# Kernel tuning notes

Hardware: AMD Instinct MI355X
Metric: run time of the kernel (lower is better)

The kernel has to match this reference:

```python
import jax, jax.numpy as jnp
import numpy as np

B, S, D_MODEL, N_HEADS = 4, 2048, 1024, 16
HEAD = D_MODEL // N_HEADS  # 64


def setup_inputs() -> dict:
    key = jax.random.key(0)
    ks = jax.random.split(key, 9)
    s = 1.0 / np.sqrt(D_MODEL)
    return {
        "query": jax.random.normal(ks[0], (B, S, D_MODEL), jnp.float32),
        "key_in": jax.random.normal(ks[1], (B, S, D_MODEL), jnp.float32),
        "value": jax.random.normal(ks[2], (B, S, D_MODEL), jnp.float32),
        "Wq": jax.random.normal(ks[3], (D_MODEL, D_MODEL), jnp.float32) * s,
        "bq": jnp.zeros((D_MODEL,), jnp.float32),
        "Wk": jax.random.normal(ks[4], (D_MODEL, D_MODEL), jnp.float32) * s,
        "bk": jnp.zeros((D_MODEL,), jnp.float32),
        "Wv": jax.random.normal(ks[5], (D_MODEL, D_MODEL), jnp.float32) * s,
        "bv": jnp.zeros((D_MODEL,), jnp.float32),
    }


def reference(query, key_in, value, Wq, bq, Wk, bk, Wv, bv):
    # Dense projections (Keras Dense: x @ W + b)
    q = query @ Wq + bq     # [B,S,D]
    k = key_in @ Wk + bk    # [B,S,D]
    v = value @ Wv + bv     # [B,S,D]
    # split heads -> [B,S,H,Dh]
    q = q.reshape(B, S, N_HEADS, HEAD)
    k = k.reshape(B, S, N_HEADS, HEAD)
    v = v.reshape(B, S, N_HEADS, HEAD)
    scale = 1.0 / jnp.sqrt(jnp.float32(HEAD))
    # full attention matrix [B,H,Sq,Sk] (faithful to original un-fused form)
    scores = jnp.einsum('bqhd,bkhd->bhqk', q, k) * scale
    alpha = jax.nn.softmax(scores, axis=-1)
    ctx = jnp.einsum('bhqk,bkhd->bqhd', alpha, v)  # [B,Sq,H,Dh]
    return ctx.reshape(B, S, D_MODEL)
```

## Files before the change

kernel.cpp:

```cpp
#include <hip/hip_runtime.h>
#include <hip/hip_bf16.h>

#define S_LEN 2048
#define DM    1024
#define NH    16
#define HD    64

typedef __attribute__((ext_vector_type(8))) short short8;
typedef __attribute__((ext_vector_type(4))) short short4v;
typedef __attribute__((ext_vector_type(4))) float f32x4;

__device__ __forceinline__ short f2bf(float f) {
    union { float f; unsigned u; } x; x.f = f;
    unsigned u = x.u;
    return (short)((u + 0x7FFFu + ((u >> 16) & 1u)) >> 16);
}
__device__ __forceinline__ short f2bf_ru(float f) {
    return (short)((__float_as_uint(f) + 0x8000u) >> 16);
}
__device__ __forceinline__ unsigned pk2bf(float a, float b) {
    unsigned ua = __float_as_uint(a) + 0x8000u;
    unsigned ub = __float_as_uint(b) + 0x8000u;
    return (ua >> 16) | (ub & 0xFFFF0000u);
}
__device__ __forceinline__ float fexp2(float x) {
#if __has_builtin(__builtin_amdgcn_exp2f)
    return __builtin_amdgcn_exp2f(x);
#else
    return exp2f(x);
#endif
}
__device__ __forceinline__ void gload_lds16(const void* g, void* l) {
    __builtin_amdgcn_global_load_lds(
        (const __attribute__((address_space(1))) unsigned int*)g,
        (__attribute__((address_space(3))) unsigned int*)l, 16, 0, 0);
}

__global__ void wt_kernel(const float* __restrict__ Wq, const float* __restrict__ Wk,
                          const float* __restrict__ Wv, short* __restrict__ wt_base) {
    __shared__ float t[32][33];
    const float* W = (blockIdx.z == 0) ? Wq : (blockIdx.z == 1 ? Wk : Wv);
    short* WT = wt_base + (size_t)blockIdx.z * DM * DM;
    int kb = blockIdx.x * 32, nb = blockIdx.y * 32;
    int tx = threadIdx.x, ty = threadIdx.y;
#pragma unroll
    for (int r = 0; r < 4; r++)
        t[ty + 8 * r][tx] = W[(size_t)(kb + ty + 8 * r) * DM + nb + tx];
    __syncthreads();
#pragma unroll
    for (int r = 0; r < 4; r++)
        WT[(size_t)(nb + ty + 8 * r) * DM + kb + tx] = f2bf(t[tx][ty + 8 * r]);
}

__global__ __launch_bounds__(256, 3) void projf_kernel(
        const float* __restrict__ Xq, const float* __restrict__ Xk,
        const float* __restrict__ Xv, const short* __restrict__ WT3,
        const float* __restrict__ bq, const float* __restrict__ bk,
        const float* __restrict__ bv,
        short* __restrict__ Qh, short* __restrict__ Kh, short* __restrict__ Vt,
        float qscale) {
    __shared__ __align__(16) short As[2][128 * 32];
    __shared__ __align__(16) short Bs[2][128 * 32];
    const int z = blockIdx.z;
    const float* X = (z == 0) ? Xq : (z == 1) ? Xk : Xv;
    const short* WT = WT3 + (size_t)z * DM * DM;
    const float* bias = (z == 0) ? bq : (z == 1) ? bk : bv;
    short* out = (z == 0) ? Qh : (z == 1) ? Kh : Vt;
    const float scale = (z == 0) ? qscale : 1.0f;
    const int mode = (z == 2);

    const int tid = threadIdx.x;
    const int lane = tid & 63, w = tid >> 6;
    const int l15 = lane & 15, quad = lane >> 4;
    const int n0 = blockIdx.x * 128, m0 = blockIdx.y * 128;
    const int wm = (w & 1) * 64, wn = (w >> 1) * 64;
    const int arow = tid >> 3;
    const int ako  = (tid & 7) * 4;

    const float* xb = X + (size_t)m0 * DM;

    f32x4 acc[4][4];
#pragma unroll
    for (int i = 0; i < 4; i++)
#pragma unroll
        for (int j = 0; j < 4; j++) { acc[i][j][0] = 0.f; acc[i][j][1] = 0.f; acc[i][j][2] = 0.f; acc[i][j][3] = 0.f; }

    float4 araw[4];
#pragma unroll
    for (int it = 0; it < 4; it++)
        araw[it] = *(const float4*)(xb + (size_t)(it * 32 + arow) * DM + ako);
#pragma unroll
    for (int it = 0; it < 2; it++) {
        int c = it * 256 + tid;
        int row = c >> 2, ko = (c & 3) * 8;
        gload_lds16(WT + (size_t)(n0 + row) * DM + ko, Bs[0] + c * 8);
    }
#pragma unroll
    for (int it = 0; it < 4; it++) {
        int row = it * 32 + arow;
        uint2 p; p.x = pk2bf(araw[it].x, araw[it].y); p.y = pk2bf(araw[it].z, araw[it].w);
        *(uint2*)(As[0] + row * 32 + ako) = p;
    }

    for (int t = 0; t < 32; t++) {
        const int bi = t & 1;
        const int kn = t * 32 + 32;
        __syncthreads();

        short8 af[4], bf[4];
#pragma unroll
        for (int i = 0; i < 4; i++)
            af[i] = *(const short8*)(As[bi] + (wm + i * 16 + l15) * 32 + quad * 8);
#pragma unroll
        for (int j = 0; j < 4; j++)
            bf[j] = *(const short8*)(Bs[bi] + (wn + j * 16 + l15) * 32 + quad * 8);

        if (t < 31) {
#pragma unroll
            for (int it = 0; it < 4; it++)
                araw[it] = *(const float4*)(xb + (size_t)(it * 32 + arow) * DM + kn + ako);
#pragma unroll
            for (int it = 0; it < 2; it++) {
                int c = it * 256 + tid;
                int row = c >> 2, ko = (c & 3) * 8;
                gload_lds16(WT + (size_t)(n0 + row) * DM + kn + ko, Bs[bi ^ 1] + c * 8);
            }
        }

#pragma unroll
        for (int i = 0; i < 4; i++)
#pragma unroll
            for (int j = 0; j < 4; j++)
                acc[i][j] = __builtin_amdgcn_mfma_f32_16x16x32_bf16(af[i], bf[j], acc[i][j], 0, 0, 0);

        if (t < 31) {
#pragma unroll
            for (int it = 0; it < 4; it++) {
                int row = it * 32 + arow;
                uint2 p; p.x = pk2bf(araw[it].x, araw[it].y); p.y = pk2bf(araw[it].z, araw[it].w);
                *(uint2*)(As[bi ^ 1] + row * 32 + ako) = p;
            }
        }
    }

#pragma unroll
    for (int j = 0; j < 4; j++) {
        int col = n0 + wn + j * 16 + l15;
        float bv_ = bias[col];
        int h = col >> 6, d = col & 63;
#pragma unroll
        for (int i = 0; i < 4; i++) {
            int rowbase = m0 + wm + i * 16 + quad * 4;
            int bb = rowbase >> 11, s0 = rowbase & 2047;
            if (mode == 0) {
#pragma unroll
                for (int r = 0; r < 4; r++)
                    out[((size_t)(bb * NH + h) * S_LEN + (s0 + r)) * HD + d] =
                        f2bf((acc[i][j][r] + bv_) * scale);
            } else {
                short4v pk;
#pragma unroll
                for (int r = 0; r < 4; r++) pk[r] = f2bf((acc[i][j][r] + bv_) * scale);
                *(short4v*)(out + ((size_t)(bb * NH + h) * HD + d) * S_LEN + s0) = pk;
            }
        }
    }
}

__global__ __launch_bounds__(256, 3) void attn_kernel(
        const short* __restrict__ Q, const short* __restrict__ K,
        const short* __restrict__ V, float* __restrict__ out) {
    __shared__ __align__(16) short Ks[2][2][64][32];
    __shared__ __align__(16) short Vs[2][2][64][32];
    __shared__ __align__(16) short ps[4][2][16 * 72];
    const int tid = threadIdx.x;
    const int lane = tid & 63, w = tid >> 6;
    const int l15 = lane & 15, quad = lane >> 4;
    const int b = blockIdx.z, h = blockIdx.y;
    const int q0 = blockIdx.x * 128;
    const size_t bh = (size_t)(b * NH + h);
    const short* qp = Q + bh * S_LEN * HD;
    const short* kp = K + bh * S_LEN * HD;
    const short* vp = V + bh * (size_t)HD * S_LEN;

    const int sg_half = (tid >> 8);

    short8 qa[2][2];
#pragma unroll
    for (int s = 0; s < 2; s++) {
        const short* qr = qp + (size_t)(q0 + w * 32 + s * 16 + l15) * HD + quad * 8;
        qa[s][0] = *(const short8*)(qr);
        qa[s][1] = *(const short8*)(qr + 32);
    }

    f32x4 o[2][4];
    float lsum[2][4];
#pragma unroll
    for (int s = 0; s < 2; s++)
#pragma unroll
        for (int d = 0; d < 4; d++) {
            o[s][d][0] = 0.f; o[s][d][1] = 0.f; o[s][d][2] = 0.f; o[s][d][3] = 0.f;
            lsum[s][d] = 0.f;
        }

    auto stageKV = [&](int kt, int bi) {
        short* kd = &Ks[bi][0][0][0];
        short* vd = &Vs[bi][0][0][0];
#pragma unroll
        for (int it = 0; it < 2; it++) {
            int c = it * 256 + tid;
            int half = c >> 8, row = (c >> 2) & 63, chunk = c & 3;
            int co = half * 32 + chunk * 8;
            gload_lds16(kp + (size_t)(kt + row) * HD + co, kd + c * 8);
            gload_lds16(vp + (size_t)row * S_LEN + kt + co, vd + c * 8);
        }
    };
    (void)sg_half;

    stageKV(0, 0);

    for (int t = 0; t < 32; t++) {
        const int bi = t & 1;
        __syncthreads();
        if (t < 31) stageKV((t + 1) << 6, bi ^ 1);

        short8 kf[4][2];
#pragma unroll
        for (int nb = 0; nb < 4; nb++) {
            kf[nb][0] = *(const short8*)(&Ks[bi][0][nb * 16 + l15][quad * 8]);
            kf[nb][1] = *(const short8*)(&Ks[bi][1][nb * 16 + l15][quad * 8]);
        }
        f32x4 sacc[2][4];
#pragma unroll
        for (int nb = 0; nb < 4; nb++)
#pragma unroll
            for (int s = 0; s < 2; s++) {
                f32x4 zz; zz[0] = 0.f; zz[1] = 0.f; zz[2] = 0.f; zz[3] = 0.f;
                zz = __builtin_amdgcn_mfma_f32_16x16x32_bf16(qa[s][0], kf[nb][0], zz, 0, 0, 0);
                sacc[s][nb] = __builtin_amdgcn_mfma_f32_16x16x32_bf16(qa[s][1], kf[nb][1], zz, 0, 0, 0);
            }
#pragma unroll
        for (int s = 0; s < 2; s++)
#pragma unroll
            for (int r = 0; r < 4; r++)
#pragma unroll
                for (int nb = 0; nb < 4; nb++) {
                    float p = fexp2(sacc[s][nb][r]);
                    lsum[s][r] += p;
                    ps[w][s][(quad * 4 + r) * 72 + nb * 16 + l15] = f2bf_ru(p);
                }
        asm volatile("s_waitcnt lgkmcnt(0)" ::: "memory");
        short8 pa[2][2];
#pragma unroll
        for (int s = 0; s < 2; s++) {
            pa[s][0] = *(const short8*)(&ps[w][s][l15 * 72 + quad * 8]);
            pa[s][1] = *(const short8*)(&ps[w][s][l15 * 72 + 32 + quad * 8]);
        }
#pragma unroll
        for (int dd = 0; dd < 4; dd++) {
            short8 v0 = *(const short8*)(&Vs[bi][0][dd * 16 + l15][quad * 8]);
            short8 v1 = *(const short8*)(&Vs[bi][1][dd * 16 + l15][quad * 8]);
#pragma unroll
            for (int s = 0; s < 2; s++) {
                o[s][dd] = __builtin_amdgcn_mfma_f32_16x16x32_bf16(pa[s][0], v0, o[s][dd], 0, 0, 0);
                o[s][dd] = __builtin_amdgcn_mfma_f32_16x16x32_bf16(pa[s][1], v1, o[s][dd], 0, 0, 0);
            }
        }
    }

#pragma unroll
    for (int s = 0; s < 2; s++) {
#pragma unroll
        for (int r = 0; r < 4; r++) {
            float l = lsum[s][r];
            l += __shfl_xor(l, 1);
            l += __shfl_xor(l, 2);
            l += __shfl_xor(l, 4);
            l += __shfl_xor(l, 8);
            lsum[s][r] = 1.f / l;
        }
        float* orow = out + ((size_t)b * S_LEN + q0 + w * 32 + s * 16 + quad * 4) * DM + h * HD + l15;
#pragma unroll
        for (int r = 0; r < 4; r++)
#pragma unroll
            for (int dd = 0; dd < 4; dd++)
                orow[(size_t)r * DM + dd * 16] = o[s][dd][r] * lsum[s][r];
    }
}

extern "C" void kernel_launch(void* const* d_in, const int* in_sizes, int n_in,
                              void* d_out, int out_size, void* d_ws, size_t ws_size,
                              hipStream_t stream) {
    const float* query  = (const float*)d_in[0];
    const float* key_in = (const float*)d_in[1];
    const float* value  = (const float*)d_in[2];
    const float* Wq = (const float*)d_in[3];
    const float* bq = (const float*)d_in[4];
    const float* Wk = (const float*)d_in[5];
    const float* bk = (const float*)d_in[6];
    const float* Wv = (const float*)d_in[7];
    const float* bv = (const float*)d_in[8];

    short* wt = (short*)d_ws;
    short* Qh = wt + 3 * 1048576;
    short* Kh = Qh + 8388608;
    short* Vt = Kh + 8388608;
    float* out = (float*)d_out;

    const float QSCALE = 0.125f * 1.44269504088896340736f;

    wt_kernel<<<dim3(32, 32, 3), dim3(32, 8), 0, stream>>>(Wq, Wk, Wv, wt);
    projf_kernel<<<dim3(8, 64, 3), 256, 0, stream>>>(query, key_in, value, wt,
                                                     bq, bk, bv, Qh, Kh, Vt, QSCALE);
    attn_kernel<<<dim3(16, NH, 4), 256, 0, stream>>>(Qh, Kh, Vt, out);
}
```

Baseline: 374.7 us.

## Pre-convert inputs to bf16 for async-LDS projection; load V directly in attention

Adds a conversion kernel that turns the fp32 activations into bf16, storing two of them in the output buffer as scratch, and a new projection GEMM that stages both operands with direct global-to-LDS loads. The old fp32 projection path is kept as a fallback when the workspace is too small. In attention, V is no longer staged through shared memory: V fragments are loaded straight from global into registers, split around the softmax to hide latency, and occupancy is raised to 4 blocks. This trades an extra full pass over the inputs and uncoalesced-ish global V reads for lower LDS use and simpler GEMM staging.

```diff
diff --git a/kernel.cpp b/kernel.cpp
--- a/kernel.cpp
+++ b/kernel.cpp
@@ -50,6 +50,106 @@
 #pragma unroll
     for (int r = 0; r < 4; r++)
         WT[(size_t)(nb + ty + 8 * r) * DM + kb + tx] = f2bf(t[tx][ty + 8 * r]);
+}
+
+__global__ __launch_bounds__(256) void cvt_kernel(
+        const float* __restrict__ Xq, const float* __restrict__ Xk,
+        const float* __restrict__ Xv, short* __restrict__ Yq,
+        short* __restrict__ Yk, short* __restrict__ Yv) {
+    const int z = blockIdx.z;
+    const float* X = (z == 0) ? Xq : (z == 1) ? Xk : Xv;
+    short* Y = (z == 0) ? Yq : (z == 1) ? Yk : Yv;
+    size_t i = ((size_t)blockIdx.x * 256 + threadIdx.x) * 8;
+    float4 a = *(const float4*)(X + i);
+    float4 b = *(const float4*)(X + i + 4);
+    uint2 p0, p1;
+    p0.x = pk2bf(a.x, a.y); p0.y = pk2bf(a.z, a.w);
+    p1.x = pk2bf(b.x, b.y); p1.y = pk2bf(b.z, b.w);
+    *(uint2*)(Y + i) = p0;
+    *(uint2*)(Y + i + 4) = p1;
+}
+
+__global__ __launch_bounds__(256, 4) void projc_kernel(
+        const short* __restrict__ Xq, const short* __restrict__ Xk,
+        const short* __restrict__ Xv, const short* __restrict__ WT3,
+        const float* __restrict__ bq, const float* __restrict__ bk,
+        const float* __restrict__ bv,
+        short* __restrict__ Qh, short* __restrict__ Kh, short* __restrict__ Vt,
+        float qscale) {
+    __shared__ __align__(16) short As[2][128 * 32];
+    __shared__ __align__(16) short Bs[2][128 * 32];
+    const int z = blockIdx.z;
+    const short* X = (z == 0) ? Xq : (z == 1) ? Xk : Xv;
+    const short* WT = WT3 + (size_t)z * DM * DM;
+    const float* bias = (z == 0) ? bq : (z == 1) ? bk : bv;
+    short* out = (z == 0) ? Qh : (z == 1) ? Kh : Vt;
+    const float scale = (z == 0) ? qscale : 1.0f;
+    const int mode = (z == 2);
+
+    const int tid = threadIdx.x;
+    const int lane = tid & 63, w = tid >> 6;
+    const int l15 = lane & 15, quad = lane >> 4;
+    const int n0 = blockIdx.x * 128, m0 = blockIdx.y * 128;
+    const int wm = (w & 1) * 64, wn = (w >> 1) * 64;
+
+    f32x4 acc[4][4];
+#pragma unroll
+    for (int i = 0; i < 4; i++)
+#pragma unroll
+        for (int j = 0; j < 4; j++) { acc[i][j][0] = 0.f; acc[i][j][1] = 0.f; acc[i][j][2] = 0.f; acc[i][j][3] = 0.f; }
+
+    const int srow = tid >> 2, sko = (tid & 3) * 8;
+    auto stage = [&](int k0, int bi) {
+#pragma unroll
+        for (int it = 0; it < 2; it++) {
+            int row = it * 64 + srow;
+            gload_lds16(X  + (size_t)(m0 + row) * DM + k0 + sko, As[bi] + row * 32 + sko);
+            gload_lds16(WT + (size_t)(n0 + row) * DM + k0 + sko, Bs[bi] + row * 32 + sko);
+        }
+    };
+
+    stage(0, 0);
+    for (int t = 0; t < 32; t++) {
+        const int bi = t & 1;
+        __syncthreads();
+        if (t < 31) stage((t + 1) * 32, bi ^ 1);
+
+        short8 af[4], bf[4];
+#pragma unroll
+        for (int i = 0; i < 4; i++)
+            af[i] = *(const short8*)(As[bi] + (wm + i * 16 + l15) * 32 + quad * 8);
+#pragma unroll
+        for (int j = 0; j < 4; j++)
+            bf[j] = *(const short8*)(Bs[bi] + (wn + j * 16 + l15) * 32 + quad * 8);
+#pragma unroll
+        for (int i = 0; i < 4; i++)
+#pragma unroll
+            for (int j = 0; j < 4; j++)
+                acc[i][j] = __builtin_amdgcn_mfma_f32_16x16x32_bf16(af[i], bf[j], acc[i][j], 0, 0, 0);
+    }
+
+#pragma unroll
+    for (int j = 0; j < 4; j++) {
+        int col = n0 + wn + j * 16 + l15;
+        float bv_ = bias[col];
+        int h = col >> 6, d = col & 63;
+#pragma unroll
+        for (int i = 0; i < 4; i++) {
+            int rowbase = m0 + wm + i * 16 + quad * 4;
+            int bb = rowbase >> 11, s0 = rowbase & 2047;
+            if (mode == 0) {
+#pragma unroll
+                for (int r = 0; r < 4; r++)
+                    out[((size_t)(bb * NH + h) * S_LEN + (s0 + r)) * HD + d] =
+                        f2bf((acc[i][j][r] + bv_) * scale);
+            } else {
+                short4v pk;
+#pragma unroll
+                for (int r = 0; r < 4; r++) pk[r] = f2bf((acc[i][j][r] + bv_) * scale);
+                *(short4v*)(out + ((size_t)(bb * NH + h) * HD + d) * S_LEN + s0) = pk;
+            }
+        }
+    }
 }
 
 __global__ __launch_bounds__(256, 3) void projf_kernel(
@@ -76,7 +176,6 @@
     const int wm = (w & 1) * 64, wn = (w >> 1) * 64;
     const int arow = tid >> 3;
     const int ako  = (tid & 7) * 4;
-
     const float* xb = X + (size_t)m0 * DM;
 
     f32x4 acc[4][4];
@@ -167,11 +266,10 @@
     }
 }
 
-__global__ __launch_bounds__(256, 3) void attn_kernel(
+__global__ __launch_bounds__(256, 4) void attn_kernel(
         const short* __restrict__ Q, const short* __restrict__ K,
         const short* __restrict__ V, float* __restrict__ out) {
     __shared__ __align__(16) short Ks[2][2][64][32];
-    __shared__ __align__(16) short Vs[2][2][64][32];
     __shared__ __align__(16) short ps[4][2][16 * 72];
     const int tid = threadIdx.x;
     const int lane = tid & 63, w = tid >> 6;
@@ -183,8 +281,6 @@
     const short* kp = K + bh * S_LEN * HD;
     const short* vp = V + bh * (size_t)HD * S_LEN;
 
-    const int sg_half = (tid >> 8);
-
     short8 qa[2][2];
 #pragma unroll
     for (int s = 0; s < 2; s++) {
@@ -203,42 +299,45 @@
             lsum[s][d] = 0.f;
         }
 
-    auto stageKV = [&](int kt, int bi) {
+    auto stageK = [&](int kt, int bi) {
         short* kd = &Ks[bi][0][0][0];
-        short* vd = &Vs[bi][0][0][0];
 #pragma unroll
         for (int it = 0; it < 2; it++) {
             int c = it * 256 + tid;
             int half = c >> 8, row = (c >> 2) & 63, chunk = c & 3;
-            int co = half * 32 + chunk * 8;
-            gload_lds16(kp + (size_t)(kt + row) * HD + co, kd + c * 8);
-            gload_lds16(vp + (size_t)row * S_LEN + kt + co, vd + c * 8);
+            gload_lds16(kp + (size_t)(kt + row) * HD + half * 32 + chunk * 8, kd + c * 8);
         }
     };
-    (void)sg_half;
-
-    stageKV(0, 0);
+
+    stageK(0, 0);
 
     for (int t = 0; t < 32; t++) {
         const int bi = t & 1;
+        const int kt = t << 6;
         __syncthreads();
-        if (t < 31) stageKV((t + 1) << 6, bi ^ 1);
-
-        short8 kf[4][2];
+        if (t < 31) stageK(kt + 64, bi ^ 1);
+
+        f32x4 sacc[2][4];
 #pragma unroll
         for (int nb = 0; nb < 4; nb++) {
-            kf[nb][0] = *(const short8*)(&Ks[bi][0][nb * 16 + l15][quad * 8]);
-            kf[nb][1] = *(const short8*)(&Ks[bi][1][nb * 16 + l15][quad * 8]);
-        }
-        f32x4 sacc[2][4];
-#pragma unroll
-        for (int nb = 0; nb < 4; nb++)
+            short8 k0v = *(const short8*)(&Ks[bi][0][nb * 16 + l15][quad * 8]);
+            short8 k1v = *(const short8*)(&Ks[bi][1][nb * 16 + l15][quad * 8]);
 #pragma unroll
             for (int s = 0; s < 2; s++) {
                 f32x4 zz; zz[0] = 0.f; zz[1] = 0.f; zz[2] = 0.f; zz[3] = 0.f;
-                zz = __builtin_amdgcn_mfma_f32_16x16x32_bf16(qa[s][0], kf[nb][0], zz, 0, 0, 0);
-                sacc[s][nb] = __builtin_amdgcn_mfma_f32_16x16x32_bf16(qa[s][1], kf[nb][1], zz, 0, 0, 0);
-            }
+                zz = __builtin_amdgcn_mfma_f32_16x16x32_bf16(qa[s][0], k0v, zz, 0, 0, 0);
+                sacc[s][nb] = __builtin_amdgcn_mfma_f32_16x16x32_bf16(qa[s][1], k1v, zz, 0, 0, 0);
+            }
+        }
+
+        short8 vf0[4];
+#pragma unroll
+        for (int dd = 0; dd < 2; dd++) {
+            const short* vr = vp + (size_t)(dd * 16 + l15) * S_LEN + kt + quad * 8;
+            vf0[2 * dd]     = *(const short8*)(vr);
+            vf0[2 * dd + 1] = *(const short8*)(vr + 32);
+        }
+
 #pragma unroll
         for (int s = 0; s < 2; s++)
 #pragma unroll
@@ -249,6 +348,15 @@
                     lsum[s][r] += p;
                     ps[w][s][(quad * 4 + r) * 72 + nb * 16 + l15] = f2bf_ru(p);
                 }
+
+        short8 vf1[4];
+#pragma unroll
+        for (int dd = 0; dd < 2; dd++) {
+            const short* vr = vp + (size_t)((dd + 2) * 16 + l15) * S_LEN + kt + quad * 8;
+            vf1[2 * dd]     = *(const short8*)(vr);
+            vf1[2 * dd + 1] = *(const short8*)(vr + 32);
+        }
+
         asm volatile("s_waitcnt lgkmcnt(0)" ::: "memory");
         short8 pa[2][2];
 #pragma unroll
@@ -256,16 +364,21 @@
             pa[s][0] = *(const short8*)(&ps[w][s][l15 * 72 + quad * 8]);
             pa[s][1] = *(const short8*)(&ps[w][s][l15 * 72 + 32 + quad * 8]);
         }
-#pragma unroll
-        for (int dd = 0; dd < 4; dd++) {
-            short8 v0 = *(const short8*)(&Vs[bi][0][dd * 16 + l15][quad * 8]);
-            short8 v1 = *(const short8*)(&Vs[bi][1][dd * 16 + l15][quad * 8]);
+
+#pragma unroll
+        for (int dd = 0; dd < 2; dd++)
 #pragma unroll
             for (int s = 0; s < 2; s++) {
-                o[s][dd] = __builtin_amdgcn_mfma_f32_16x16x32_bf16(pa[s][0], v0, o[s][dd], 0, 0, 0);
-                o[s][dd] = __builtin_amdgcn_mfma_f32_16x16x32_bf16(pa[s][1], v1, o[s][dd], 0, 0, 0);
-            }
-        }
+                o[s][dd] = __builtin_amdgcn_mfma_f32_16x16x32_bf16(pa[s][0], vf0[2 * dd], o[s][dd], 0, 0, 0);
+                o[s][dd] = __builtin_amdgcn_mfma_f32_16x16x32_bf16(pa[s][1], vf0[2 * dd + 1], o[s][dd], 0, 0, 0);
+            }
+#pragma unroll
+        for (int dd = 0; dd < 2; dd++)
+#pragma unroll
+            for (int s = 0; s < 2; s++) {
+                o[s][dd + 2] = __builtin_amdgcn_mfma_f32_16x16x32_bf16(pa[s][0], vf1[2 * dd], o[s][dd + 2], 0, 0, 0);
+                o[s][dd + 2] = __builtin_amdgcn_mfma_f32_16x16x32_bf16(pa[s][1], vf1[2 * dd + 1], o[s][dd + 2], 0, 0, 0);
+            }
     }
 
 #pragma unroll
@@ -305,12 +418,23 @@
     short* Qh = wt + 3 * 1048576;
     short* Kh = Qh + 8388608;
     short* Vt = Kh + 8388608;
+    short* Xv = Vt + 8388608;
     float* out = (float*)d_out;
 
     const float QSCALE = 0.125f * 1.44269504088896340736f;
 
     wt_kernel<<<dim3(32, 32, 3), dim3(32, 8), 0, stream>>>(Wq, Wk, Wv, wt);
-    projf_kernel<<<dim3(8, 64, 3), 256, 0, stream>>>(query, key_in, value, wt,
-                                                     bq, bk, bv, Qh, Kh, Vt, QSCALE);
+
+    if (ws_size >= 73400320u) {
+        short* Xq = (short*)d_out;
+        short* Xk = Xq + 8388608;
+        cvt_kernel<<<dim3(4096, 1, 3), 256, 0, stream>>>(query, key_in, value, Xq, Xk, Xv);
+        projc_kernel<<<dim3(8, 64, 3), 256, 0, stream>>>(Xq, Xk, Xv, wt,
+                                                         bq, bk, bv, Qh, Kh, Vt, QSCALE);
+    } else {
+        projf_kernel<<<dim3(8, 64, 3), 256, 0, stream>>>(query, key_in, value, wt,
+                                                         bq, bk, bv, Qh, Kh, Vt, QSCALE);
+    }
+
     attn_kernel<<<dim3(16, NH, 4), 256, 0, stream>>>(Qh, Kh, Vt, out);
 }
```

Result: no change. 376.8 us (+0.5%).
